# Kernel optimization log

Measured on AMD Instinct MI355X. Metric: run time of the kernel, lower is better.

## Reference

```python
import jax, jax.numpy as jnp
import numpy as np

B, D_IN, H, NZ, NC = 32768, 768, 2048, 128, 1024
EPS, NITERS = 0.5, 15


def setup_inputs() -> dict:
    key = jax.random.key(0)
    ks = jax.random.split(key, 4)
    x = jax.random.normal(ks[0], (B, D_IN), jnp.float32)
    # scaled init so feature magnitudes keep exp(-dist/eps) in f32 range
    W1 = jax.random.normal(ks[1], (D_IN, H), jnp.float32) / np.sqrt(D_IN)
    b1 = jnp.zeros((H,), jnp.float32)
    W2 = jax.random.normal(ks[2], (H, NZ), jnp.float32) / np.sqrt(H)
    b2 = jnp.zeros((NZ,), jnp.float32)
    centroids = jax.random.normal(ks[3], (NC, NZ), jnp.float32)
    return {
        'x': x, 'W1': W1, 'b1': b1, 'W2': W2, 'b2': b2,
        'centroids': centroids,
        'cluster_counts': jnp.zeros((NC,), jnp.int32),
        'raw_counts': jnp.zeros((NC,), jnp.int32),
        'total_soft_counts': jnp.zeros((NC,), jnp.float32),
    }


def _sinkhorn(scores, eps=EPS, niters=NITERS):
    # scores: [B, K].  Q: [K, B], matches torch reference where sum(Q) = col-sums.
    Q = jnp.exp(scores / eps).T
    Q = Q / jnp.sum(Q, axis=0, keepdims=True)
    K, Bb = Q.shape
    r = 1.0 / K
    c = 1.0 / Bb

    def body(Q, _):
        Q = Q * (r / jnp.sum(Q, axis=1))[:, None]
        Q = Q * (c / jnp.sum(Q, axis=0))[None, :]
        return Q, None

    Q, _ = jax.lax.scan(body, Q, None, length=niters)
    return (Q / jnp.sum(Q, axis=0, keepdims=True)).T  # [B, K]


def reference(x, W1, b1, W2, b2, centroids, cluster_counts, raw_counts, total_soft_counts):
    # fc backbone: Linear -> ReLU -> Linear
    fv = jax.nn.relu(x @ W1 + b1) @ W2 + b2                        # [B, nz]
    # pairwise euclidean distances to centroids (cdist via gram trick;
    # avoids materializing the [B, nc, nz] broadcast torch creates)
    sq = (jnp.sum(fv * fv, axis=1)[:, None]
          + jnp.sum(centroids * centroids, axis=1)[None, :]
          - 2.0 * fv @ centroids.T)
    cluster_dists = jnp.sqrt(jnp.maximum(sq, 1e-12))               # [B, nc]

    # sinkhorn branch (no_grad in torch)
    soft_assignments = jax.lax.stop_gradient(_sinkhorn(-cluster_dists))
    batch_assignments = jnp.argmin(soft_assignments, axis=1)       # [B]
    soft_counts = jnp.sum(soft_assignments, axis=0)                # [nc]
    # soft_train=False: gather assigned distances
    loss = jnp.mean(jnp.take_along_axis(cluster_dists, batch_assignments[:, None], axis=1))

    # scatter-accumulate counts
    new_raw = raw_counts.at[jnp.argmin(cluster_dists, axis=1)].add(1)
    new_cluster = cluster_counts.at[batch_assignments].add(1)
    new_total_soft = total_soft_counts + soft_counts
    return loss, batch_assignments, soft_counts, new_raw, new_cluster, new_total_soft
```

## Files before the change

### kernel.cpp

```cpp
#include <hip/hip_runtime.h>
#include <math.h>

#define BN    32768
#define DIN   768
#define HN    2048
#define NZ    128
#define NCN   1024

typedef __attribute__((ext_vector_type(8))) short s16x8;
typedef __attribute__((ext_vector_type(4))) float f32x4;
typedef unsigned short u16;

#define MFMA16(a,b,c) __builtin_amdgcn_mfma_f32_16x16x32_bf16(a,b,c,0,0,0)

__device__ __forceinline__ u16 bf16_rne(float x){
  unsigned u = __float_as_uint(x);
  unsigned r = (u + 0x7FFFu + ((u >> 16) & 1u)) >> 16;
  return (u16)r;
}
__device__ __forceinline__ float bf16_tof(u16 h){
  return __uint_as_float(((unsigned)h) << 16);
}
__device__ __forceinline__ void split3(float x, u16& h, u16& m, u16& l){
  h = bf16_rne(x);
  float r1 = x - bf16_tof(h);
  m = bf16_rne(r1);
  float r2 = r1 - bf16_tof(m);
  l = bf16_rne(r2);
}

__device__ __forceinline__ void gload16(const void* gsrc, void* lds){
  __builtin_amdgcn_global_load_lds(
      (const __attribute__((address_space(1))) unsigned int*)gsrc,
      (__attribute__((address_space(3))) unsigned int*)lds, 16, 0, 0);
}

__global__ __launch_bounds__(1024) void k0_init(float* u, int* hraw, int* hclu){
  const int k = threadIdx.x;
  u[k] = 1.0f;
  hraw[k] = 0;
  hclu[k] = 0;
}

__global__ __launch_bounds__(256) void c_split(
    const float* __restrict__ in, u16* __restrict__ oh, u16* __restrict__ om,
    u16* __restrict__ ol, int n4)
{
  const int i = blockIdx.x*256 + threadIdx.x;
  if (i >= n4) return;
  const f32x4 v = *(const f32x4*)&in[(size_t)i*4];
  ushort4 h4, m4, l4;
  split3(v[0], h4.x, m4.x, l4.x);
  split3(v[1], h4.y, m4.y, l4.y);
  split3(v[2], h4.z, m4.z, l4.z);
  split3(v[3], h4.w, m4.w, l4.w);
  *(ushort4*)&oh[(size_t)i*4] = h4;
  *(ushort4*)&om[(size_t)i*4] = m4;
  *(ushort4*)&ol[(size_t)i*4] = l4;
}

__global__ __launch_bounds__(256) void c_tsplit(
    const float* __restrict__ in, int R, int C,
    u16* __restrict__ oh, u16* __restrict__ om, u16* __restrict__ ol)
{
  __shared__ float L[64][65];
  const int t = threadIdx.x;
  const int bi = blockIdx.x, bj = blockIdx.y;
  #pragma unroll
  for (int m=0;m<4;++m){
    int flat = t + 256*m;
    int r = flat >> 4, c4 = (flat & 15) << 2;
    const float4 v = *(const float4*)&in[(size_t)(bi*64 + r)*C + bj*64 + c4];
    L[r][c4+0] = v.x; L[r][c4+1] = v.y; L[r][c4+2] = v.z; L[r][c4+3] = v.w;
  }
  __syncthreads();
  #pragma unroll
  for (int m=0;m<4;++m){
    int flat = t + 256*m;
    int oc = flat >> 4, k4 = (flat & 15) << 2;
    ushort4 h4, m4, l4;
    split3(L[k4+0][oc], h4.x, m4.x, l4.x);
    split3(L[k4+1][oc], h4.y, m4.y, l4.y);
    split3(L[k4+2][oc], h4.z, m4.z, l4.z);
    split3(L[k4+3][oc], h4.w, m4.w, l4.w);
    size_t off = (size_t)(bj*64 + oc)*R + bi*64 + k4;
    *(ushort4*)&oh[off] = h4;
    *(ushort4*)&om[off] = m4;
    *(ushort4*)&ol[off] = l4;
  }
}

__global__ __launch_bounds__(256) void c_norm(
    const float* __restrict__ in, float* __restrict__ out)
{
  const int w = threadIdx.x >> 6, l = threadIdx.x & 63;
  const int row = blockIdx.x*4 + w;
  const float2 v = *(const float2*)&in[(size_t)row*128 + l*2];
  float s = v.x*v.x + v.y*v.y;
  #pragma unroll
  for (int off=32; off; off>>=1) s += __shfl_xor(s, off, 64);
  if (l == 0) out[row] = s;
}

__global__ __launch_bounds__(256, 2) void k1_mfma(
    const u16* __restrict__ Xh, const u16* __restrict__ Xm, const u16* __restrict__ Xl,
    const u16* __restrict__ W1h, const u16* __restrict__ W1m, const u16* __restrict__ W1l,
    const float* __restrict__ b1,
    const u16* __restrict__ W2h, const u16* __restrict__ W2m, const u16* __restrict__ W2l,
    const float* __restrict__ b2, float* __restrict__ fv)
{
  __shared__ __align__(16) unsigned char sm[73728];
  unsigned char* xsr = sm;
  unsigned char* wsr = sm + 24576;

  const int t  = threadIdx.x;
  const int l  = t & 63;
  const int wn = t >> 6;
  const int g  = (l >> 4) & 3;
  const int lr = l & 15;
  const int bid = blockIdx.x;
  const int swz = (bid & 7)*64 + (bid >> 3);
  const int row0 = swz * 64;

  f32x4 fvacc[4][2];
  #pragma unroll
  for (int mf=0;mf<4;++mf){
    fvacc[mf][0] = (f32x4){0.f,0.f,0.f,0.f};
    fvacc[mf][1] = (f32x4){0.f,0.f,0.f,0.f};
  }

  #pragma unroll 1
  for (int nc = 0; nc < 16; ++nc){
    f32x4 a1acc[4][2];
    #pragma unroll
    for (int mf=0;mf<4;++mf){
      a1acc[mf][0] = (f32x4){0.f,0.f,0.f,0.f};
      a1acc[mf][1] = (f32x4){0.f,0.f,0.f,0.f};
    }

    #pragma unroll 1
    for (int ks = 0; ks < 12; ++ks){
      #pragma unroll
      for (int i=0;i<6;++i){
        const int ci = wn*6 + i;
        const int s  = ci >> 3;
        const int rb = ci & 7;
        const int xr = rb*8 + (l >> 3);
        const int q  = l & 7;
        const u16* Xp = (s==0) ? Xh : ((s==1) ? Xm : Xl);
        const u16* src = Xp + (size_t)(row0 + xr)*768 + ks*64 + ((q ^ (xr & 7)) << 3);
        gload16(src, xsr + s*8192 + rb*1024);
      }
      #pragma unroll
      for (int i=0;i<12;++i){
        const int ci = wn*12 + i;
        const int s  = ci >> 4;
        const int rb = ci & 15;
        const int rloc = rb*8 + (l >> 3);
        const int q  = l & 7;
        const u16* Wp = (s==0) ? W1h : ((s==1) ? W1m : W1l);
        const u16* src = Wp + (size_t)(nc*128 + rloc)*768 + ks*64 + ((q ^ (rloc & 7)) << 3);
        gload16(src, wsr + s*16384 + rb*1024);
      }
      __syncthreads();

      #pragma unroll
      for (int kk=0;kk<2;++kk){
        s16x8 Bf[3][2], Af[3][4];
        #pragma unroll
        for (int s=0;s<3;++s){
          #pragma unroll
          for (int nf=0;nf<2;++nf){
            const int br = wn*32 + nf*16 + lr;
            Bf[s][nf] = *(const s16x8*)(wsr + s*16384 + br*128 + ((16*(g + 4*kk)) ^ ((br & 7) << 4)));
          }
          #pragma unroll
          for (int mf=0;mf<4;++mf){
            const int ar = mf*16 + lr;
            Af[s][mf] = *(const s16x8*)(xsr + s*8192 + ar*128 + ((16*(g + 4*kk)) ^ ((ar & 7) << 4)));
          }
        }
        #pragma unroll
        for (int mf=0;mf<4;++mf){
          #pragma unroll
          for (int nf=0;nf<2;++nf){
            f32x4 acc = a1acc[mf][nf];
            acc = MFMA16(Af[0][mf], Bf[0][nf], acc);
            acc = MFMA16(Af[0][mf], Bf[1][nf], acc);
            acc = MFMA16(Af[1][mf], Bf[0][nf], acc);
            acc = MFMA16(Af[1][mf], Bf[1][nf], acc);
            acc = MFMA16(Af[0][mf], Bf[2][nf], acc);
            acc = MFMA16(Af[2][mf], Bf[0][nf], acc);
            a1acc[mf][nf] = acc;
          }
        }
      }
      __syncthreads();
    }

    const float b1v0 = b1[nc*128 + wn*32 + lr];
    const float b1v1 = b1[nc*128 + wn*32 + 16 + lr];

    #pragma unroll
    for (int half=0; half<2; ++half){
      if ((wn >> 1) == half){
        #pragma unroll
        for (int mf=0;mf<4;++mf){
          #pragma unroll
          for (int nf=0;nf<2;++nf){
            const int klocal = (wn & 1)*32 + nf*16 + lr;
            #pragma unroll
            for (int r=0;r<4;++r){
              float vv = a1acc[mf][nf][r] + ((nf==0) ? b1v0 : b1v1);
              vv = vv > 0.f ? vv : 0.f;
              u16 sh, sm2, sl;
              split3(vv, sh, sm2, sl);
              const int ar = mf*16 + g*4 + r;
              const int bo = ar*128 + ((2*klocal) ^ ((ar & 7) << 4));
              *(u16*)(xsr + bo)         = sh;
              *(u16*)(xsr + 8192 + bo)  = sm2;
              *(u16*)(xsr + 16384 + bo) = sl;
            }
          }
        }
      }
      #pragma unroll
      for (int i=0;i<12;++i){
        const int ci = wn*12 + i;
        const int s  = ci >> 4;
        const int rb = ci & 15;
        const int rloc = rb*8 + (l >> 3);
        const int q  = l & 7;
        const u16* Wp = (s==0) ? W2h : ((s==1) ? W2m : W2l);
        const u16* src = Wp + (size_t)rloc*2048 + nc*128 + half*64 + ((q ^ (rloc & 7)) << 3);
        gload16(src, wsr + s*16384 + rb*1024);
      }
      __syncthreads();

      #pragma unroll
      for (int kk=0;kk<2;++kk){
        s16x8 Bf[3][2], Af[3][4];
        #pragma unroll
        for (int s=0;s<3;++s){
          #pragma unroll
          for (int nf=0;nf<2;++nf){
            const int br = wn*32 + nf*16 + lr;
            Bf[s][nf] = *(const s16x8*)(wsr + s*16384 + br*128 + ((16*(g + 4*kk)) ^ ((br & 7) << 4)));
          }
          #pragma unroll
          for (int mf=0;mf<4;++mf){
            const int ar = mf*16 + lr;
            Af[s][mf] = *(const s16x8*)(xsr + s*8192 + ar*128 + ((16*(g + 4*kk)) ^ ((ar & 7) << 4)));
          }
        }
        #pragma unroll
        for (int mf=0;mf<4;++mf){
          #pragma unroll
          for (int nf=0;nf<2;++nf){
            f32x4 acc = fvacc[mf][nf];
            acc = MFMA16(Af[0][mf], Bf[0][nf], acc);
            acc = MFMA16(Af[0][mf], Bf[1][nf], acc);
            acc = MFMA16(Af[1][mf], Bf[0][nf], acc);
            acc = MFMA16(Af[1][mf], Bf[1][nf], acc);
            acc = MFMA16(Af[0][mf], Bf[2][nf], acc);
            acc = MFMA16(Af[2][mf], Bf[0][nf], acc);
            fvacc[mf][nf] = acc;
          }
        }
      }
      __syncthreads();
    }
  }

  const float b2v0 = b2[wn*32 + lr];
  const float b2v1 = b2[wn*32 + 16 + lr];
  #pragma unroll
  for (int mf=0;mf<4;++mf){
    #pragma unroll
    for (int nf=0;nf<2;++nf){
      #pragma unroll
      for (int r=0;r<4;++r){
        const int frow = row0 + mf*16 + g*4 + r;
        const int col  = wn*32 + nf*16 + lr;
        fv[(size_t)frow*NZ + col] = fvacc[mf][nf][r] + ((nf==0) ? b2v0 : b2v1);
      }
    }
  }
}

__global__ __launch_bounds__(256, 2) void k2_mfma(
    const u16* __restrict__ fvh, const u16* __restrict__ fvm, const u16* __restrict__ fvl,
    const u16* __restrict__ ch,  const u16* __restrict__ cm,  const u16* __restrict__ cl,
    const float* __restrict__ fvn, const float* __restrict__ cn,
    float* __restrict__ Q0)
{
  __shared__ __align__(16) unsigned char bs[49152];
  __shared__ float cnl[NCN];
  const int t  = threadIdx.x;
  const int l  = t & 63;
  const int wn = t >> 6;
  const int g  = (l >> 4) & 3;
  const int lr = l & 15;
  const int bid = blockIdx.x;
  const int swz = (bid & 7)*64 + (bid >> 3);
  const int row0 = swz * 64;
  const int arow = row0 + wn*16 + lr;

  s16x8 Af[3][4];
  #pragma unroll
  for (int kk=0;kk<4;++kk){
    const size_t ao = (size_t)arow*128 + kk*32 + g*8;
    Af[0][kk] = *(const s16x8*)&fvh[ao];
    Af[1][kk] = *(const s16x8*)&fvm[ao];
    Af[2][kk] = *(const s16x8*)&fvl[ao];
  }
  #pragma unroll
  for (int m=0;m<4;++m) cnl[t + 256*m] = cn[t + 256*m];
  const f32x4 fvnv = *(const f32x4*)&fvn[row0 + wn*16 + g*4];

  #pragma unroll 1
  for (int cc = 0; cc < NCN; cc += 64){
    #pragma unroll
    for (int i=0;i<12;++i){
      const int ci = wn*12 + i;
      const int s  = ci >> 4;
      const int rb = ci & 15;
      const int crow = rb*4 + (l >> 4);
      const int q  = l & 15;
      const u16* Cp = (s==0) ? ch : ((s==1) ? cm : cl);
      const u16* src = Cp + (size_t)(cc + crow)*128 + ((q ^ (crow & 15)) << 3);
      gload16(src, bs + s*16384 + rb*1024);
    }
    __syncthreads();

    f32x4 acc[4];
    #pragma unroll
    for (int nf=0;nf<4;++nf) acc[nf] = (f32x4){0.f,0.f,0.f,0.f};

    #pragma unroll
    for (int kk=0;kk<4;++kk){
      s16x8 Bq[3][4];
      #pragma unroll
      for (int nf=0;nf<4;++nf){
        const int br = nf*16 + lr;
        const int base = br*256 + (((g + 4*kk) ^ (br & 15)) << 4);
        Bq[0][nf] = *(const s16x8*)(bs + base);
        Bq[1][nf] = *(const s16x8*)(bs + 16384 + base);
        Bq[2][nf] = *(const s16x8*)(bs + 32768 + base);
      }
      #pragma unroll
      for (int nf=0;nf<4;++nf){
        f32x4 a = acc[nf];
        a = MFMA16(Af[0][kk], Bq[0][nf], a);
        a = MFMA16(Af[0][kk], Bq[1][nf], a);
        a = MFMA16(Af[1][kk], Bq[0][nf], a);
        a = MFMA16(Af[1][kk], Bq[1][nf], a);
        a = MFMA16(Af[0][kk], Bq[2][nf], a);
        a = MFMA16(Af[2][kk], Bq[0][nf], a);
        acc[nf] = a;
      }
    }

    #pragma unroll
    for (int nf=0;nf<4;++nf){
      const int n = cc + nf*16 + lr;
      const float cv = cnl[n];
      #pragma unroll
      for (int r=0;r<4;++r){
        float sq = fvnv[r] + cv - 2.0f*acc[nf][r];
        sq = sq > 1e-12f ? sq : 1e-12f;
        const float d = sqrtf(sq);
        Q0[(size_t)(row0 + wn*16 + g*4 + r)*NCN + n] = expf(-2.0f*d);
      }
    }
    __syncthreads();
  }
}

__global__ __launch_bounds__(256, 2) void k3_pass(
    const float* __restrict__ Q0, const float* __restrict__ u,
    float* __restrict__ S_part, float alpha)
{
  __shared__ __align__(16) float Sw[4][NCN];
  const int t = threadIdx.x;
  const int w = t >> 6, l = t & 63;

  f32x4 uu[4], sacc[4];
  #pragma unroll
  for (int j=0;j<4;++j){
    uu[j] = *(const f32x4*)&u[4*(l + 64*j)];
    sacc[j] = (f32x4){0.f,0.f,0.f,0.f};
  }

  const int gw = blockIdx.x*4 + w;
  const size_t b0 = (size_t)gw * 16;
  #pragma unroll 1
  for (int rr=0; rr<16; rr+=4){
    f32x4 q[4][4];
    float part[4];
    #pragma unroll
    for (int rq=0;rq<4;++rq){
      const f32x4* qrow = (const f32x4*)(Q0 + (b0 + rr + rq)*NCN);
      float p = 0.f;
      #pragma unroll
      for (int j=0;j<4;++j){
        q[rq][j] = qrow[l + 64*j];
        p += q[rq][j][0]*uu[j][0]; p += q[rq][j][1]*uu[j][1];
        p += q[rq][j][2]*uu[j][2]; p += q[rq][j][3]*uu[j][3];
      }
      part[rq] = p;
    }
    #pragma unroll
    for (int off=32; off; off>>=1){
      #pragma unroll
      for (int rq=0;rq<4;++rq) part[rq] += __shfl_xor(part[rq], off, 64);
    }
    #pragma unroll
    for (int rq=0;rq<4;++rq){
      const float v = alpha / part[rq];
      #pragma unroll
      for (int j=0;j<4;++j){
        sacc[j][0] += q[rq][j][0]*v; sacc[j][1] += q[rq][j][1]*v;
        sacc[j][2] += q[rq][j][2]*v; sacc[j][3] += q[rq][j][3]*v;
      }
    }
  }
  #pragma unroll
  for (int j=0;j<4;++j) *(f32x4*)&Sw[w][4*(l + 64*j)] = sacc[j];
  __syncthreads();
  #pragma unroll
  for (int m=0;m<4;++m){
    int k = t + 256*m;
    S_part[(size_t)blockIdx.x*NCN + k] = ((Sw[0][k]+Sw[1][k])+(Sw[2][k]+Sw[3][k]));
  }
}

__global__ __launch_bounds__(256) void k4_unew(
    const float* __restrict__ S_part, float* __restrict__ u)
{
  __shared__ float P[256];
  const int t = threadIdx.x;
  const int c = t & 15;
  const int seg = t >> 4;
  const int col = blockIdx.x*16 + c;
  float p = 0.f;
  #pragma unroll 4
  for (int i=0;i<32;++i)
    p += S_part[(size_t)(seg*32 + i)*NCN + col];
  P[seg*16 + c] = p;
  __syncthreads();
  #pragma unroll
  for (int s2=8; s2>0; s2>>=1){
    if (seg < s2) P[seg*16 + c] += P[(seg+s2)*16 + c];
    __syncthreads();
  }
  if (seg == 0) u[col] = (1.0f/1024.0f) / P[c];
}

__global__ __launch_bounds__(256, 2) void k5_final(
    const float* __restrict__ Q0, const float* __restrict__ u,
    float* __restrict__ softc_part, float* __restrict__ loss_part,
    int* __restrict__ hist_raw, int* __restrict__ hist_clu,
    float* __restrict__ out_ba)
{
  __shared__ __align__(16) float Sw[4][NCN];
  __shared__ float lossw[4];
  const int t = threadIdx.x;
  const int w = t >> 6, l = t & 63;

  f32x4 uu[4], sacc[4];
  #pragma unroll
  for (int j=0;j<4;++j){
    uu[j] = *(const f32x4*)&u[4*(l + 64*j)];
    sacc[j] = (f32x4){0.f,0.f,0.f,0.f};
  }

  const int gw = blockIdx.x*4 + w;
  const size_t b0 = (size_t)gw * 16;
  float lacc = 0.f;
  #pragma unroll 1
  for (int rr=0; rr<16; ++rr){
    const size_t b = b0 + rr;
    const f32x4* qrow = (const f32x4*)(Q0 + b*NCN);
    f32x4 q4[4], wv4[4];
    float part = 0.f;
    #pragma unroll
    for (int j=0;j<4;++j){
      q4[j] = qrow[l + 64*j];
      wv4[j][0] = uu[j][0]*q4[j][0]; wv4[j][1] = uu[j][1]*q4[j][1];
      wv4[j][2] = uu[j][2]*q4[j][2]; wv4[j][3] = uu[j][3]*q4[j][3];
      part += wv4[j][0]; part += wv4[j][1]; part += wv4[j][2]; part += wv4[j][3];
    }
    #pragma unroll
    for (int off=32; off; off>>=1) part += __shfl_xor(part, off, 64);
    const float inv = 1.0f / part;

    float smin = wv4[0][0] * inv; int kmin = 4*l; float qat = q4[0][0];
    float qmax = q4[0][0];        int kmax = 4*l;
    #pragma unroll
    for (int j=0;j<4;++j){
      #pragma unroll
      for (int c=0;c<4;++c){
        if (j==0 && c==0) continue;
        const float qv = q4[j][c];
        const float sv = wv4[j][c] * inv;
        const int k = 4*(l + 64*j) + c;
        if (sv < smin){ smin = sv; kmin = k; qat = qv; }
        if (qv > qmax){ qmax = qv; kmax = k; }
      }
    }
    #pragma unroll
    for (int off=32; off; off>>=1){
      float s2 = __shfl_xor(smin, off, 64);
      int   k2 = __shfl_xor(kmin, off, 64);
      float q2 = __shfl_xor(qat,  off, 64);
      if (s2 < smin || (s2 == smin && k2 < kmin)){ smin=s2; kmin=k2; qat=q2; }
      float m2 = __shfl_xor(qmax, off, 64);
      int   i2 = __shfl_xor(kmax, off, 64);
      if (m2 > qmax || (m2 == qmax && i2 < kmax)){ qmax=m2; kmax=i2; }
    }
    #pragma unroll
    for (int j=0;j<4;++j){
      sacc[j][0] += wv4[j][0]*inv; sacc[j][1] += wv4[j][1]*inv;
      sacc[j][2] += wv4[j][2]*inv; sacc[j][3] += wv4[j][3]*inv;
    }
    if (l == 0){
      out_ba[b] = (float)kmin;
      atomicAdd(&hist_clu[kmin], 1);
      atomicAdd(&hist_raw[kmax], 1);
      lacc += -0.5f * logf(qat);
    }
  }
  #pragma unroll
  for (int j=0;j<4;++j) *(f32x4*)&Sw[w][4*(l + 64*j)] = sacc[j];
  if (l == 0) lossw[w] = lacc;
  __syncthreads();
  #pragma unroll
  for (int m=0;m<4;++m){
    int k = t + 256*m;
    softc_part[(size_t)blockIdx.x*NCN + k] = ((Sw[0][k]+Sw[1][k])+(Sw[2][k]+Sw[3][k]));
  }
  if (t == 0) loss_part[blockIdx.x] = ((lossw[0]+lossw[1])+(lossw[2]+lossw[3]));
}

__global__ __launch_bounds__(1024) void k6_fin(
    const float* __restrict__ softc_part, const float* __restrict__ loss_part,
    const int* __restrict__ hist_raw, const int* __restrict__ hist_clu,
    const int* __restrict__ raw_in, const int* __restrict__ clu_in,
    const float* __restrict__ tsoft_in, float* __restrict__ out)
{
  const int k = threadIdx.x;
  float s0=0.f,s1=0.f,s2=0.f,s3=0.f;
  for (int blk=0; blk<512; blk+=4){
    s0 += softc_part[(size_t)(blk+0)*NCN + k];
    s1 += softc_part[(size_t)(blk+1)*NCN + k];
    s2 += softc_part[(size_t)(blk+2)*NCN + k];
    s3 += softc_part[(size_t)(blk+3)*NCN + k];
  }
  const float s = ((s0+s1)+(s2+s3));
  out[1 + BN + k]           = s;
  out[1 + BN + NCN + k]     = (float)(raw_in[k] + hist_raw[k]);
  out[1 + BN + 2*NCN + k]   = (float)(clu_in[k] + hist_clu[k]);
  out[1 + BN + 3*NCN + k]   = tsoft_in[k] + s;
  if (k == 0){
    float ls = 0.f;
    for (int i=0;i<512;++i) ls += loss_part[i];
    out[0] = ls / 32768.0f;
  }
}

extern "C" void kernel_launch(void* const* d_in, const int* in_sizes, int n_in,
                              void* d_out, int out_size, void* d_ws, size_t ws_size,
                              hipStream_t stream) {
  (void)in_sizes; (void)n_in; (void)out_size; (void)ws_size;
  const float* x      = (const float*)d_in[0];
  const float* W1     = (const float*)d_in[1];
  const float* b1     = (const float*)d_in[2];
  const float* W2     = (const float*)d_in[3];
  const float* b2     = (const float*)d_in[4];
  const float* cent   = (const float*)d_in[5];
  const int*   clu_in = (const int*)d_in[6];
  const int*   raw_in = (const int*)d_in[7];
  const float* tsoft  = (const float*)d_in[8];
  float* out = (float*)d_out;

  float* ws        = (float*)d_ws;
  float* fv        = ws;
  float* Q0        = ws + 4194304;
  u16*   Xh        = (u16*)Q0;
  u16*   Xm        = Xh + 25165824;
  u16*   Xl        = Xm + 25165824;
  float* softc_par = ws + 37748736;
  float* loss_par  = softc_par + 524288;
  float* u         = ws + 41943040;
  float* S_part    = u + 1024;
  int*   hist_raw  = (int*)(S_part + 524288);
  int*   hist_clu  = hist_raw + 1024;
  float* wbase     = (float*)(hist_clu + 1024);
  u16* W1Th = (u16*)wbase;
  u16* W1Tm = W1Th + 1572864;
  u16* W1Tl = W1Tm + 1572864;
  u16* W2Th = W1Tl + 1572864;
  u16* W2Tm = W2Th + 262144;
  u16* W2Tl = W2Tm + 262144;
  u16* fvh = (u16*)wbase;
  u16* fvm = fvh + 4194304;
  u16* fvl = fvm + 4194304;
  u16* ch  = fvl + 4194304;
  u16* cm  = ch  + 131072;
  u16* cl  = cm  + 131072;
  float* fvn = wbase + 6488064;
  float* cn  = fvn + 32768;
  float* out_ba = out + 1;

  c_split <<<24576, 256, 0, stream>>>(x, Xh, Xm, Xl, 6291456);
  c_tsplit<<<dim3(12, 32), 256, 0, stream>>>(W1, 768, 2048, W1Th, W1Tm, W1Tl);
  c_tsplit<<<dim3(32, 2),  256, 0, stream>>>(W2, 2048, 128, W2Th, W2Tm, W2Tl);
  k0_init<<<1, 1024, 0, stream>>>(u, hist_raw, hist_clu);

  k1_mfma<<<512, 256, 0, stream>>>(Xh, Xm, Xl, W1Th, W1Tm, W1Tl, b1,
                                   W2Th, W2Tm, W2Tl, b2, fv);

  c_split<<<4096, 256, 0, stream>>>(fv,   fvh, fvm, fvl, 1048576);
  c_split<<<128,  256, 0, stream>>>(cent, ch,  cm,  cl,  32768);
  c_norm <<<8192, 256, 0, stream>>>(fv,   fvn);
  c_norm <<<256,  256, 0, stream>>>(cent, cn);

  k2_mfma<<<512, 256, 0, stream>>>(fvh, fvm, fvl, ch, cm, cl, fvn, cn, Q0);

  for (int it = 0; it < 15; ++it){
    const float alpha = (it == 0) ? 1.0f : (1.0f/32768.0f);
    k3_pass<<<512, 256, 0, stream>>>(Q0, u, S_part, alpha);
    k4_unew<<<64, 256, 0, stream>>>(S_part, u);
  }
  k5_final<<<512, 256, 0, stream>>>(Q0, u, softc_par, loss_par,
                                    hist_raw, hist_clu, out_ba);
  k6_fin<<<1, 1024, 0, stream>>>(softc_par, loss_par, hist_raw, hist_clu,
                                 raw_in, clu_in, tsoft, out);
}
```

Measured before the change: 1.283 ms.

## Fuse Sinkhorn iterations and finalization into one cooperative persistent kernel

Replaces the 30 alternating k3_pass/k4_unew launches plus k5_final and k6_fin with a single cooperative kernel that uses grid-wide syncs between phases. The u vector stays in registers across iterations and the column-sum reduction is spread over all 512 blocks, removing per-launch overhead and idle gaps between small kernels. In exchange it requires all 512 blocks to be co-resident (two per CU at 256 threads) and adds grid barrier costs and agent-scope atomic loads.

```diff
diff --git a/kernel.cpp b/kernel.cpp
--- a/kernel.cpp
+++ b/kernel.cpp
@@ -1,5 +1,8 @@
 #include <hip/hip_runtime.h>
+#include <hip/hip_cooperative_groups.h>
 #include <math.h>
+
+namespace cg = cooperative_groups;
 
 #define BN    32768
 #define DIN   768
@@ -35,9 +38,18 @@
       (__attribute__((address_space(3))) unsigned int*)lds, 16, 0, 0);
 }
 
-__global__ __launch_bounds__(1024) void k0_init(float* u, int* hraw, int* hclu){
+__device__ __forceinline__ float agload(const float* p){
+  return __hip_atomic_load(p, __ATOMIC_RELAXED, __HIP_MEMORY_SCOPE_AGENT);
+}
+__device__ __forceinline__ int agloadi(const int* p){
+  return __hip_atomic_load(p, __ATOMIC_RELAXED, __HIP_MEMORY_SCOPE_AGENT);
+}
+__device__ __forceinline__ void agstore(float* p, float v){
+  __hip_atomic_store(p, v, __ATOMIC_RELAXED, __HIP_MEMORY_SCOPE_AGENT);
+}
+
+__global__ __launch_bounds__(1024) void k0_init(int* hraw, int* hclu){
   const int k = threadIdx.x;
-  u[k] = 1.0f;
   hraw[k] = 0;
   hclu[k] = 0;
 }
@@ -377,195 +389,211 @@
   }
 }
 
-__global__ __launch_bounds__(256, 2) void k3_pass(
-    const float* __restrict__ Q0, const float* __restrict__ u,
-    float* __restrict__ S_part, float alpha)
-{
-  __shared__ __align__(16) float Sw[4][NCN];
-  const int t = threadIdx.x;
-  const int w = t >> 6, l = t & 63;
-
-  f32x4 uu[4], sacc[4];
-  #pragma unroll
-  for (int j=0;j<4;++j){
-    uu[j] = *(const f32x4*)&u[4*(l + 64*j)];
-    sacc[j] = (f32x4){0.f,0.f,0.f,0.f};
-  }
-
-  const int gw = blockIdx.x*4 + w;
-  const size_t b0 = (size_t)gw * 16;
-  #pragma unroll 1
-  for (int rr=0; rr<16; rr+=4){
-    f32x4 q[4][4];
-    float part[4];
-    #pragma unroll
-    for (int rq=0;rq<4;++rq){
-      const f32x4* qrow = (const f32x4*)(Q0 + (b0 + rr + rq)*NCN);
-      float p = 0.f;
-      #pragma unroll
-      for (int j=0;j<4;++j){
-        q[rq][j] = qrow[l + 64*j];
-        p += q[rq][j][0]*uu[j][0]; p += q[rq][j][1]*uu[j][1];
-        p += q[rq][j][2]*uu[j][2]; p += q[rq][j][3]*uu[j][3];
-      }
-      part[rq] = p;
-    }
-    #pragma unroll
-    for (int off=32; off; off>>=1){
-      #pragma unroll
-      for (int rq=0;rq<4;++rq) part[rq] += __shfl_xor(part[rq], off, 64);
-    }
-    #pragma unroll
-    for (int rq=0;rq<4;++rq){
-      const float v = alpha / part[rq];
-      #pragma unroll
-      for (int j=0;j<4;++j){
-        sacc[j][0] += q[rq][j][0]*v; sacc[j][1] += q[rq][j][1]*v;
-        sacc[j][2] += q[rq][j][2]*v; sacc[j][3] += q[rq][j][3]*v;
-      }
-    }
-  }
-  #pragma unroll
-  for (int j=0;j<4;++j) *(f32x4*)&Sw[w][4*(l + 64*j)] = sacc[j];
-  __syncthreads();
-  #pragma unroll
-  for (int m=0;m<4;++m){
-    int k = t + 256*m;
-    S_part[(size_t)blockIdx.x*NCN + k] = ((Sw[0][k]+Sw[1][k])+(Sw[2][k]+Sw[3][k]));
-  }
-}
-
-__global__ __launch_bounds__(256) void k4_unew(
-    const float* __restrict__ S_part, float* __restrict__ u)
-{
-  __shared__ float P[256];
-  const int t = threadIdx.x;
-  const int c = t & 15;
-  const int seg = t >> 4;
-  const int col = blockIdx.x*16 + c;
-  float p = 0.f;
-  #pragma unroll 4
-  for (int i=0;i<32;++i)
-    p += S_part[(size_t)(seg*32 + i)*NCN + col];
-  P[seg*16 + c] = p;
-  __syncthreads();
-  #pragma unroll
-  for (int s2=8; s2>0; s2>>=1){
-    if (seg < s2) P[seg*16 + c] += P[(seg+s2)*16 + c];
-    __syncthreads();
-  }
-  if (seg == 0) u[col] = (1.0f/1024.0f) / P[c];
-}
-
-__global__ __launch_bounds__(256, 2) void k5_final(
-    const float* __restrict__ Q0, const float* __restrict__ u,
+__global__ __launch_bounds__(256, 2) void k35_coop(
+    const float* __restrict__ Q0, float* __restrict__ S_part,
+    float* __restrict__ ug,
     float* __restrict__ softc_part, float* __restrict__ loss_part,
     int* __restrict__ hist_raw, int* __restrict__ hist_clu,
-    float* __restrict__ out_ba)
-{
-  __shared__ __align__(16) float Sw[4][NCN];
-  __shared__ float lossw[4];
-  const int t = threadIdx.x;
-  const int w = t >> 6, l = t & 63;
-
-  f32x4 uu[4], sacc[4];
-  #pragma unroll
-  for (int j=0;j<4;++j){
-    uu[j] = *(const f32x4*)&u[4*(l + 64*j)];
-    sacc[j] = (f32x4){0.f,0.f,0.f,0.f};
-  }
-
-  const int gw = blockIdx.x*4 + w;
-  const size_t b0 = (size_t)gw * 16;
-  float lacc = 0.f;
-  #pragma unroll 1
-  for (int rr=0; rr<16; ++rr){
-    const size_t b = b0 + rr;
-    const f32x4* qrow = (const f32x4*)(Q0 + b*NCN);
-    f32x4 q4[4], wv4[4];
-    float part = 0.f;
-    #pragma unroll
-    for (int j=0;j<4;++j){
-      q4[j] = qrow[l + 64*j];
-      wv4[j][0] = uu[j][0]*q4[j][0]; wv4[j][1] = uu[j][1]*q4[j][1];
-      wv4[j][2] = uu[j][2]*q4[j][2]; wv4[j][3] = uu[j][3]*q4[j][3];
-      part += wv4[j][0]; part += wv4[j][1]; part += wv4[j][2]; part += wv4[j][3];
-    }
-    #pragma unroll
-    for (int off=32; off; off>>=1) part += __shfl_xor(part, off, 64);
-    const float inv = 1.0f / part;
-
-    float smin = wv4[0][0] * inv; int kmin = 4*l; float qat = q4[0][0];
-    float qmax = q4[0][0];        int kmax = 4*l;
-    #pragma unroll
-    for (int j=0;j<4;++j){
-      #pragma unroll
-      for (int c=0;c<4;++c){
-        if (j==0 && c==0) continue;
-        const float qv = q4[j][c];
-        const float sv = wv4[j][c] * inv;
-        const int k = 4*(l + 64*j) + c;
-        if (sv < smin){ smin = sv; kmin = k; qat = qv; }
-        if (qv > qmax){ qmax = qv; kmax = k; }
-      }
-    }
-    #pragma unroll
-    for (int off=32; off; off>>=1){
-      float s2 = __shfl_xor(smin, off, 64);
-      int   k2 = __shfl_xor(kmin, off, 64);
-      float q2 = __shfl_xor(qat,  off, 64);
-      if (s2 < smin || (s2 == smin && k2 < kmin)){ smin=s2; kmin=k2; qat=q2; }
-      float m2 = __shfl_xor(qmax, off, 64);
-      int   i2 = __shfl_xor(kmax, off, 64);
-      if (m2 > qmax || (m2 == qmax && i2 < kmax)){ qmax=m2; kmax=i2; }
-    }
-    #pragma unroll
-    for (int j=0;j<4;++j){
-      sacc[j][0] += wv4[j][0]*inv; sacc[j][1] += wv4[j][1]*inv;
-      sacc[j][2] += wv4[j][2]*inv; sacc[j][3] += wv4[j][3]*inv;
-    }
-    if (l == 0){
-      out_ba[b] = (float)kmin;
-      atomicAdd(&hist_clu[kmin], 1);
-      atomicAdd(&hist_raw[kmax], 1);
-      lacc += -0.5f * logf(qat);
-    }
-  }
-  #pragma unroll
-  for (int j=0;j<4;++j) *(f32x4*)&Sw[w][4*(l + 64*j)] = sacc[j];
-  if (l == 0) lossw[w] = lacc;
-  __syncthreads();
-  #pragma unroll
-  for (int m=0;m<4;++m){
-    int k = t + 256*m;
-    softc_part[(size_t)blockIdx.x*NCN + k] = ((Sw[0][k]+Sw[1][k])+(Sw[2][k]+Sw[3][k]));
-  }
-  if (t == 0) loss_part[blockIdx.x] = ((lossw[0]+lossw[1])+(lossw[2]+lossw[3]));
-}
-
-__global__ __launch_bounds__(1024) void k6_fin(
-    const float* __restrict__ softc_part, const float* __restrict__ loss_part,
-    const int* __restrict__ hist_raw, const int* __restrict__ hist_clu,
+    float* __restrict__ out_ba,
     const int* __restrict__ raw_in, const int* __restrict__ clu_in,
     const float* __restrict__ tsoft_in, float* __restrict__ out)
 {
-  const int k = threadIdx.x;
-  float s0=0.f,s1=0.f,s2=0.f,s3=0.f;
-  for (int blk=0; blk<512; blk+=4){
-    s0 += softc_part[(size_t)(blk+0)*NCN + k];
-    s1 += softc_part[(size_t)(blk+1)*NCN + k];
-    s2 += softc_part[(size_t)(blk+2)*NCN + k];
-    s3 += softc_part[(size_t)(blk+3)*NCN + k];
-  }
-  const float s = ((s0+s1)+(s2+s3));
-  out[1 + BN + k]           = s;
-  out[1 + BN + NCN + k]     = (float)(raw_in[k] + hist_raw[k]);
-  out[1 + BN + 2*NCN + k]   = (float)(clu_in[k] + hist_clu[k]);
-  out[1 + BN + 3*NCN + k]   = tsoft_in[k] + s;
-  if (k == 0){
-    float ls = 0.f;
-    for (int i=0;i<512;++i) ls += loss_part[i];
-    out[0] = ls / 32768.0f;
+  __shared__ __align__(16) float Sw[4][NCN];
+  __shared__ float red[256];
+  __shared__ float lossw[4];
+  cg::grid_group grid = cg::this_grid();
+
+  const int t = threadIdx.x;
+  const int w = t >> 6, l = t & 63;
+  const int bid = blockIdx.x;
+  const int gw = bid*4 + w;
+  const size_t b0 = (size_t)gw * 16;
+
+  f32x4 uu[4];
+  #pragma unroll
+  for (int j=0;j<4;++j) uu[j] = (f32x4){1.f,1.f,1.f,1.f};
+
+  #pragma unroll 1
+  for (int it=0; it<15; ++it){
+    const float alpha = (it==0) ? 1.0f : (1.0f/32768.0f);
+    f32x4 sacc[4];
+    #pragma unroll
+    for (int j=0;j<4;++j) sacc[j] = (f32x4){0.f,0.f,0.f,0.f};
+
+    #pragma unroll 1
+    for (int rr=0; rr<16; rr+=4){
+      f32x4 q[4][4];
+      float part[4];
+      #pragma unroll
+      for (int rq=0;rq<4;++rq){
+        const f32x4* qrow = (const f32x4*)(Q0 + (b0 + rr + rq)*NCN);
+        float p = 0.f;
+        #pragma unroll
+        for (int j=0;j<4;++j){
+          q[rq][j] = qrow[l + 64*j];
+          p += q[rq][j][0]*uu[j][0]; p += q[rq][j][1]*uu[j][1];
+          p += q[rq][j][2]*uu[j][2]; p += q[rq][j][3]*uu[j][3];
+        }
+        part[rq] = p;
+      }
+      #pragma unroll
+      for (int off=32; off; off>>=1){
+        #pragma unroll
+        for (int rq=0;rq<4;++rq) part[rq] += __shfl_xor(part[rq], off, 64);
+      }
+      #pragma unroll
+      for (int rq=0;rq<4;++rq){
+        const float v = alpha / part[rq];
+        #pragma unroll
+        for (int j=0;j<4;++j){
+          sacc[j][0] += q[rq][j][0]*v; sacc[j][1] += q[rq][j][1]*v;
+          sacc[j][2] += q[rq][j][2]*v; sacc[j][3] += q[rq][j][3]*v;
+        }
+      }
+    }
+    #pragma unroll
+    for (int j=0;j<4;++j) *(f32x4*)&Sw[w][4*(l + 64*j)] = sacc[j];
+    __syncthreads();
+    #pragma unroll
+    for (int m=0;m<4;++m){
+      const int k = t + 256*m;
+      S_part[(size_t)bid*NCN + k] = ((Sw[0][k]+Sw[1][k])+(Sw[2][k]+Sw[3][k]));
+    }
+    __threadfence();
+    grid.sync();
+
+    {
+      const int c = t >> 7;
+      const int i = t & 127;
+      const int col = bid*2 + c;
+      float p0 = agload(&S_part[(size_t)(i*4+0)*NCN + col]);
+      float p1 = agload(&S_part[(size_t)(i*4+1)*NCN + col]);
+      float p2 = agload(&S_part[(size_t)(i*4+2)*NCN + col]);
+      float p3 = agload(&S_part[(size_t)(i*4+3)*NCN + col]);
+      red[t] = (p0+p1)+(p2+p3);
+      __syncthreads();
+      #pragma unroll
+      for (int s2=64; s2>0; s2>>=1){
+        if (i < s2) red[t] += red[t + s2];
+        __syncthreads();
+      }
+      if (i == 0) agstore(&ug[col], (1.0f/1024.0f) / red[c*128]);
+    }
+    __threadfence();
+    grid.sync();
+
+    #pragma unroll
+    for (int j=0;j<4;++j){
+      #pragma unroll
+      for (int c=0;c<4;++c) uu[j][c] = agload(&ug[4*(l + 64*j) + c]);
+    }
+  }
+
+  {
+    f32x4 sacc[4];
+    #pragma unroll
+    for (int j=0;j<4;++j) sacc[j] = (f32x4){0.f,0.f,0.f,0.f};
+    float lacc = 0.f;
+
+    #pragma unroll 1
+    for (int rr=0; rr<16; ++rr){
+      const size_t b = b0 + rr;
+      const f32x4* qrow = (const f32x4*)(Q0 + b*NCN);
+      f32x4 q4[4], wv4[4];
+      float part = 0.f;
+      #pragma unroll
+      for (int j=0;j<4;++j){
+        q4[j] = qrow[l + 64*j];
+        wv4[j][0] = uu[j][0]*q4[j][0]; wv4[j][1] = uu[j][1]*q4[j][1];
+        wv4[j][2] = uu[j][2]*q4[j][2]; wv4[j][3] = uu[j][3]*q4[j][3];
+        part += wv4[j][0]; part += wv4[j][1]; part += wv4[j][2]; part += wv4[j][3];
+      }
+      #pragma unroll
+      for (int off=32; off; off>>=1) part += __shfl_xor(part, off, 64);
+      const float inv = 1.0f / part;
+
+      float smin = wv4[0][0] * inv; int kmin = 4*l; float qat = q4[0][0];
+      float qmax = q4[0][0];        int kmax = 4*l;
+      #pragma unroll
+      for (int j=0;j<4;++j){
+        #pragma unroll
+        for (int c=0;c<4;++c){
+          if (j==0 && c==0) continue;
+          const float qv = q4[j][c];
+          const float sv = wv4[j][c] * inv;
+          const int k = 4*(l + 64*j) + c;
+          if (sv < smin){ smin = sv; kmin = k; qat = qv; }
+          if (qv > qmax){ qmax = qv; kmax = k; }
+        }
+      }
+      #pragma unroll
+      for (int off=32; off; off>>=1){
+        float s2 = __shfl_xor(smin, off, 64);
+        int   k2 = __shfl_xor(kmin, off, 64);
+        float q2 = __shfl_xor(qat,  off, 64);
+        if (s2 < smin || (s2 == smin && k2 < kmin)){ smin=s2; kmin=k2; qat=q2; }
+        float m2 = __shfl_xor(qmax, off, 64);
+        int   i2 = __shfl_xor(kmax, off, 64);
+        if (m2 > qmax || (m2 == qmax && i2 < kmax)){ qmax=m2; kmax=i2; }
+      }
+      #pragma unroll
+      for (int j=0;j<4;++j){
+        sacc[j][0] += wv4[j][0]*inv; sacc[j][1] += wv4[j][1]*inv;
+        sacc[j][2] += wv4[j][2]*inv; sacc[j][3] += wv4[j][3]*inv;
+      }
+      if (l == 0){
+        out_ba[b] = (float)kmin;
+        atomicAdd(&hist_clu[kmin], 1);
+        atomicAdd(&hist_raw[kmax], 1);
+        lacc += -0.5f * logf(qat);
+      }
+    }
+    #pragma unroll
+    for (int j=0;j<4;++j) *(f32x4*)&Sw[w][4*(l + 64*j)] = sacc[j];
+    if (l == 0) lossw[w] = lacc;
+    __syncthreads();
+    #pragma unroll
+    for (int m=0;m<4;++m){
+      const int k = t + 256*m;
+      softc_part[(size_t)bid*NCN + k] = ((Sw[0][k]+Sw[1][k])+(Sw[2][k]+Sw[3][k]));
+    }
+    if (t == 0) loss_part[bid] = ((lossw[0]+lossw[1])+(lossw[2]+lossw[3]));
+  }
+  __threadfence();
+  grid.sync();
+
+  if (bid < 64){
+    const int c = t & 15;
+    const int seg = t >> 4;
+    const int col = bid*16 + c;
+    float p = 0.f;
+    #pragma unroll 4
+    for (int i=0;i<32;++i)
+      p += agload(&softc_part[(size_t)(seg*32 + i)*NCN + col]);
+    red[seg*16 + c] = p;
+    __syncthreads();
+    #pragma unroll
+    for (int s2=8; s2>0; s2>>=1){
+      if (seg < s2) red[seg*16 + c] += red[(seg+s2)*16 + c];
+      __syncthreads();
+    }
+    if (seg == 0){
+      const float s = red[c];
+      out[1 + BN + col]         = s;
+      out[1 + BN + NCN + col]   = (float)(raw_in[col] + agloadi(&hist_raw[col]));
+      out[1 + BN + 2*NCN + col] = (float)(clu_in[col] + agloadi(&hist_clu[col]));
+      out[1 + BN + 3*NCN + col] = tsoft_in[col] + s;
+    }
+  } else if (bid == 64){
+    float p = agload(&loss_part[t]) + agload(&loss_part[t + 256]);
+    red[t] = p;
+    __syncthreads();
+    #pragma unroll
+    for (int s2=128; s2>0; s2>>=1){
+      if (t < s2) red[t] += red[t + s2];
+      __syncthreads();
+    }
+    if (t == 0) out[0] = red[0] / 32768.0f;
   }
 }
 
@@ -616,7 +644,7 @@
   c_split <<<24576, 256, 0, stream>>>(x, Xh, Xm, Xl, 6291456);
   c_tsplit<<<dim3(12, 32), 256, 0, stream>>>(W1, 768, 2048, W1Th, W1Tm, W1Tl);
   c_tsplit<<<dim3(32, 2),  256, 0, stream>>>(W2, 2048, 128, W2Th, W2Tm, W2Tl);
-  k0_init<<<1, 1024, 0, stream>>>(u, hist_raw, hist_clu);
+  k0_init<<<1, 1024, 0, stream>>>(hist_raw, hist_clu);
 
   k1_mfma<<<512, 256, 0, stream>>>(Xh, Xm, Xl, W1Th, W1Tm, W1Tl, b1,
                                    W2Th, W2Tm, W2Tl, b2, fv);
@@ -628,13 +656,13 @@
 
   k2_mfma<<<512, 256, 0, stream>>>(fvh, fvm, fvl, ch, cm, cl, fvn, cn, Q0);
 
-  for (int it = 0; it < 15; ++it){
-    const float alpha = (it == 0) ? 1.0f : (1.0f/32768.0f);
-    k3_pass<<<512, 256, 0, stream>>>(Q0, u, S_part, alpha);
-    k4_unew<<<64, 256, 0, stream>>>(S_part, u);
-  }
-  k5_final<<<512, 256, 0, stream>>>(Q0, u, softc_par, loss_par,
-                                    hist_raw, hist_clu, out_ba);
-  k6_fin<<<1, 1024, 0, stream>>>(softc_par, loss_par, hist_raw, hist_clu,
-                                 raw_in, clu_in, tsoft, out);
-}
+  {
+    const float* Q0c = Q0;
+    void* kargs[] = { (void*)&Q0c, (void*)&S_part, (void*)&u,
+                      (void*)&softc_par, (void*)&loss_par,
+                      (void*)&hist_raw, (void*)&hist_clu, (void*)&out_ba,
+                      (void*)&raw_in, (void*)&clu_in, (void*)&tsoft, (void*)&out };
+    hipLaunchCooperativeKernel((void*)k35_coop, dim3(512), dim3(256),
+                               kargs, 0, stream);
+  }
+}
```

New measurement: 4.380 ms. +241.3%, slower.
